# Kernel optimization log

Measured on AMD Instinct MI355X. Metric: run time of the kernel, lower is better.

## Reference

```python
import jax, jax.numpy as jnp
import numpy as np

B, C, W, H = 32, 64, 96, 96
L = 32          # LSTM hidden size
OUT = 256       # conv output channels
EPS = 1e-5


def _lstm_dir(x, wih, whh, b):
    # x: [N, T, D]; wih: [4L, D]; whh: [4L, L]; b: [4L] (b_ih + b_hh)
    N, T, D = x.shape
    Lh = whh.shape[1]
    xg = jnp.einsum('ntd,gd->ntg', x, wih) + b  # precompute input projections

    def step(carry, xg_t):
        h, c = carry
        g = xg_t + h @ whh.T
        i, f, gg, o = jnp.split(g, 4, axis=-1)  # PyTorch gate order i,f,g,o
        i = jax.nn.sigmoid(i)
        f = jax.nn.sigmoid(f)
        gg = jnp.tanh(gg)
        o = jax.nn.sigmoid(o)
        c = f * c + i * gg
        h = o * jnp.tanh(c)
        return (h, c), h

    init = (jnp.zeros((N, Lh), x.dtype), jnp.zeros((N, Lh), x.dtype))
    _, hs = jax.lax.scan(step, init, jnp.swapaxes(xg, 0, 1))
    return jnp.swapaxes(hs, 0, 1)  # [N, T, L]


def _bilstm(x, wih_f, whh_f, bih_f, bhh_f, wih_b, whh_b, bih_b, bhh_b):
    hf = _lstm_dir(x, wih_f, whh_f, bih_f + bhh_f)
    hb = _lstm_dir(x[:, ::-1], wih_b, whh_b, bih_b + bhh_b)[:, ::-1]
    return jnp.concatenate([hf, hb], axis=-1)  # [N, T, 2L]


def setup_inputs() -> dict:
    key = jax.random.key(0)
    ks = jax.random.split(key, 24)
    s1 = 1.0 / np.sqrt(L)
    def u(k, shape):
        return jax.random.uniform(k, shape, jnp.float32, -s1, s1)
    inp = {'x': jax.random.normal(ks[0], (B, C, W, H), jnp.float32)}
    # vertical LSTM: input_size=C
    inp['v_wih_f'] = u(ks[1], (4 * L, C)); inp['v_whh_f'] = u(ks[2], (4 * L, L))
    inp['v_bih_f'] = u(ks[3], (4 * L,));  inp['v_bhh_f'] = u(ks[4], (4 * L,))
    inp['v_wih_b'] = u(ks[5], (4 * L, C)); inp['v_whh_b'] = u(ks[6], (4 * L, L))
    inp['v_bih_b'] = u(ks[7], (4 * L,));  inp['v_bhh_b'] = u(ks[8], (4 * L,))
    # horizontal LSTM: input_size=2L
    inp['h_wih_f'] = u(ks[9], (4 * L, 2 * L)); inp['h_whh_f'] = u(ks[10], (4 * L, L))
    inp['h_bih_f'] = u(ks[11], (4 * L,));      inp['h_bhh_f'] = u(ks[12], (4 * L,))
    inp['h_wih_b'] = u(ks[13], (4 * L, 2 * L)); inp['h_whh_b'] = u(ks[14], (4 * L, L))
    inp['h_bih_b'] = u(ks[15], (4 * L,));       inp['h_bhh_b'] = u(ks[16], (4 * L,))
    # 1x1 conv + BN
    inp['conv_w'] = jax.random.normal(ks[17], (OUT, 2 * L), jnp.float32) * 0.05
    inp['conv_b'] = jnp.zeros((OUT,), jnp.float32)
    inp['bn_g'] = jnp.ones((OUT,), jnp.float32)
    inp['bn_b'] = jnp.zeros((OUT,), jnp.float32)
    return inp


def reference(x, v_wih_f, v_whh_f, v_bih_f, v_bhh_f, v_wih_b, v_whh_b, v_bih_b, v_bhh_b,
              h_wih_f, h_whh_f, h_bih_f, h_bhh_f, h_wih_b, h_whh_b, h_bih_b, h_bhh_b,
              conv_w, conv_b, bn_g, bn_b):
    b, c, w, h = x.shape
    xt = jnp.transpose(x, (0, 3, 2, 1))  # [B, H, W, C] (torch transpose(1,3))
    # vertical pass: for each column w, LSTM over H -> batch all columns at once
    xv = jnp.transpose(xt, (0, 2, 1, 3)).reshape(b * w, h, c)  # [B*W, H, C]
    hv = _bilstm(xv, v_wih_f, v_whh_f, v_bih_f, v_bhh_f,
                 v_wih_b, v_whh_b, v_bih_b, v_bhh_b)            # [B*W, H, 2L]
    v = jnp.transpose(hv.reshape(b, w, h, 2 * L), (0, 2, 1, 3))  # [B, H, W, 2L]
    # horizontal pass: for each row h, LSTM over W -> batch all rows at once
    xh = v.reshape(b * h, w, 2 * L)
    hh = _bilstm(xh, h_wih_f, h_whh_f, h_bih_f, h_bhh_f,
                 h_wih_b, h_whh_b, h_bih_b, h_bhh_b).reshape(b, h, w, 2 * L)
    # stack(dim=3) then transpose(1,2) in torch == [B, 2L, W, H]
    y = jnp.transpose(hh, (0, 3, 2, 1))  # [B, 2L, W, H]
    # 1x1 conv
    y = jnp.einsum('bcwh,oc->bowh', y, conv_w) + conv_b[None, :, None, None]
    # BatchNorm2d (training mode: batch statistics, biased variance)
    mean = jnp.mean(y, axis=(0, 2, 3), keepdims=True)
    var = jnp.mean((y - mean) ** 2, axis=(0, 2, 3), keepdims=True)
    out = (y - mean) * jax.lax.rsqrt(var + EPS)
    out = out * bn_g[None, :, None, None] + bn_b[None, :, None, None]
    return out
```

## Files before the change

kernel.cpp:

```cpp
#include <hip/hip_runtime.h>
#include <stdint.h>

#define DI __device__ __forceinline__

constexpr int Bn = 32, Cc = 64, Wn = 96, Hn = 96, Ln = 32, NG = 128, OUTC = 256;
constexpr int SEQ = 96;
constexpr long long NPIX = (long long)Bn * Wn * Hn;
constexpr int GRAM_BLOCKS = 256;
constexpr int PIX_PER_BLOCK = (int)(NPIX / GRAM_BLOCKS);

typedef __attribute__((ext_vector_type(8))) short bf16x8;
typedef __attribute__((ext_vector_type(4))) float f32x4;

constexpr float LOG2E  = 1.44269504088896340736f;
constexpr float TWOL2E = 2.88539008177792681472f;

DI float exp2_(float x) { return __builtin_amdgcn_exp2f(x); }
DI float rcp_(float x)  { return __builtin_amdgcn_rcpf(x); }
DI float bf2f(unsigned short u) { return __uint_as_float(((unsigned)u) << 16); }
DI unsigned short f2bf(float f) {
    unsigned u = __float_as_uint(f);
    u += 0x7FFFu + ((u >> 16) & 1u);
    return (unsigned short)(u >> 16);
}

__global__ __launch_bounds__(256)
void transpose_x(const float* __restrict__ x, unsigned short* __restrict__ xT)
{
    __shared__ alignas(16) unsigned char xs[96 * 128];
    const int tid = threadIdx.x;
    const int b = blockIdx.x / 96, q = blockIdx.x % 96;
    for (int i = tid; i < 1536; i += 256) {
        int c = i / 24, h4 = i - c * 24;
        float4 v = *(const float4*)(x + (((size_t)b * 64 + c) * 96 + q) * 96 + 4 * h4);
        float vv[4] = {v.x, v.y, v.z, v.w};
#pragma unroll
        for (int j = 0; j < 4; ++j) {
            int h = 4 * h4 + j;
            *(unsigned short*)(xs + h * 128 + ((c * 2) ^ ((h & 7) << 4))) = f2bf(vv[j]);
        }
    }
    __syncthreads();
    unsigned short* ob = xT + (size_t)blockIdx.x * 6144;
    for (int i = tid; i < 768; i += 256) {
        int row = i >> 3, k8 = i & 7;
        bf16x8 p = *(const bf16x8*)(xs + row * 128 + ((k8 * 16) ^ ((row & 7) << 4)));
        *(bf16x8*)(ob + (size_t)i * 8) = p;
    }
}

#define FLOAD(XA, XB, STI)                                                     \
    if ((STI) < 96) {                                                          \
        const int tl_ = dir ? 95 - (STI) : (STI);                              \
        XA = *(const bf16x8*)(xTb + (size_t)tl_ * 64);                         \
        XB = *(const bf16x8*)(xTb + (size_t)tl_ * 64 + 32);                    \
    }

#define PPROJ(XA, XB)                                                          \
    _Pragma("unroll")                                                          \
    for (int g_ = 0; g_ < 4; ++g_) {                                           \
        f32x4 tp_ = __builtin_amdgcn_mfma_f32_16x16x32_bf16(ax0[g_], XA, bc[g_], 0, 0, 0); \
        xac[g_] = __builtin_amdgcn_mfma_f32_16x16x32_bf16(ax1[g_], XB, tp_, 0, 0, 0);      \
    }

#define RSTEP(STI)                                                             \
    {                                                                          \
        const bf16x8 hu = *(const bf16x8*)(hcur + n_ * 80 + rg * 16);          \
        f32x4 ac_[4];                                                          \
        _Pragma("unroll")                                                      \
        for (int g_ = 0; g_ < 4; ++g_)                                         \
            ac_[g_] = __builtin_amdgcn_mfma_f32_16x16x32_bf16(ah[g_], hu, xac[g_], 0, 0, 0); \
        unsigned short hs[4];                                                  \
        _Pragma("unroll")                                                      \
        for (int j = 0; j < 4; ++j) {                                          \
            const float iv = rcp_(1.f + exp2_(-ac_[0][j]));                    \
            const float fv = rcp_(1.f + exp2_(-ac_[1][j]));                    \
            const float gr = rcp_(1.f + exp2_(-ac_[2][j]));                    \
            const float gv = fmaf(2.f, gr, -1.f);                              \
            const float ov = rcp_(1.f + exp2_(-ac_[3][j]));                    \
            cc[j] = fmaf(fv, cc[j], iv * gv);                                  \
            const float r_ = rcp_(exp2_(cc[j] * TWOL2E) + 1.f);                \
            const float t2 = -2.f * ov;                                        \
            hs[j] = f2bf(fmaf(t2, r_, ov));                                    \
        }                                                                      \
        ushort4 hp; hp.x = hs[0]; hp.y = hs[1]; hp.z = hs[2]; hp.w = hs[3];    \
        *(ushort4*)(hnxt + n_ * 80 + wv * 32 + rg * 8) = hp;                   \
        *(ushort4*)optr = hp;                                                  \
        optr += odelta;                                                        \
        __syncthreads();                                                       \
        { unsigned char* t_ = hcur; hcur = hnxt; hnxt = t_; }                  \
    }

template<int VERT>
__global__ __launch_bounds__(128, 1)
void lstm_fused(const unsigned short* __restrict__ xT,
                const float* __restrict__ wih_f, const float* __restrict__ whh_f,
                const float* __restrict__ bih_f, const float* __restrict__ bhh_f,
                const float* __restrict__ wih_b, const float* __restrict__ whh_b,
                const float* __restrict__ bih_b, const float* __restrict__ bhh_b,
                unsigned short* __restrict__ outU)
{
    __shared__ alignas(16) unsigned char hbuf[2][16 * 80];

    const int tid = threadIdx.x;
    const int wv = tid >> 6, lane = tid & 63;
    const int dir = blockIdx.x & 1, group = blockIdx.x >> 1;
    const int n_ = lane & 15, rg = lane >> 4;
    const int chain = group * 16 + n_;
    const int b = group / 6;
    const int q = (group % 6) * 16 + n_;

    const float* wih = dir ? wih_b : wih_f;
    const float* whh = dir ? whh_b : whh_f;
    const float* bih = dir ? bih_b : bih_f;
    const float* bhh = dir ? bhh_b : bhh_f;

    bf16x8 ah[4], ax0[4], ax1[4];
    f32x4 bc[4];
#pragma unroll
    for (int g_ = 0; g_ < 4; ++g_) {
        const int tt = 2 * g_ + wv;
        const float sc = (g_ == 2) ? TWOL2E : LOG2E;
        const float* sh = whh + (size_t)(tt * 16 + n_) * 32 + rg * 8;
        const float* sx = wih + (size_t)(tt * 16 + n_) * 64 + rg * 8;
        float4 h0 = *(const float4*)sh, h1 = *(const float4*)(sh + 4);
        float4 x0 = *(const float4*)sx, x1 = *(const float4*)(sx + 4);
        float4 x2 = *(const float4*)(sx + 32), x3 = *(const float4*)(sx + 36);
        ah[g_][0] = (short)f2bf(sc * h0.x); ah[g_][1] = (short)f2bf(sc * h0.y);
        ah[g_][2] = (short)f2bf(sc * h0.z); ah[g_][3] = (short)f2bf(sc * h0.w);
        ah[g_][4] = (short)f2bf(sc * h1.x); ah[g_][5] = (short)f2bf(sc * h1.y);
        ah[g_][6] = (short)f2bf(sc * h1.z); ah[g_][7] = (short)f2bf(sc * h1.w);
        ax0[g_][0] = (short)f2bf(sc * x0.x); ax0[g_][1] = (short)f2bf(sc * x0.y);
        ax0[g_][2] = (short)f2bf(sc * x0.z); ax0[g_][3] = (short)f2bf(sc * x0.w);
        ax0[g_][4] = (short)f2bf(sc * x1.x); ax0[g_][5] = (short)f2bf(sc * x1.y);
        ax0[g_][6] = (short)f2bf(sc * x1.z); ax0[g_][7] = (short)f2bf(sc * x1.w);
        ax1[g_][0] = (short)f2bf(sc * x2.x); ax1[g_][1] = (short)f2bf(sc * x2.y);
        ax1[g_][2] = (short)f2bf(sc * x2.z); ax1[g_][3] = (short)f2bf(sc * x2.w);
        ax1[g_][4] = (short)f2bf(sc * x3.x); ax1[g_][5] = (short)f2bf(sc * x3.y);
        ax1[g_][6] = (short)f2bf(sc * x3.z); ax1[g_][7] = (short)f2bf(sc * x3.w);
#pragma unroll
        for (int j = 0; j < 4; ++j) {
            const int g = tt * 16 + rg * 4 + j;
            bc[g_][j] = sc * (bih[g] + bhh[g]);
        }
    }

    const unsigned short* xTb = xT + (size_t)chain * 6144 + rg * 8;

    const int t0 = dir ? 95 : 0;
    const size_t o0 = VERT ? ((((size_t)b * 96 + t0) * 96 + q) * 64)
                           : ((((size_t)b * 96 + q) * 96 + t0) * 64);
    unsigned short* optr = outU + o0 + dir * 32 + wv * 16 + rg * 4;
    const ptrdiff_t odelta = (ptrdiff_t)(dir ? -1 : 1) * (VERT ? 6144 : 64);

    for (int i = tid; i < 320; i += 128) ((unsigned*)hbuf[0])[i] = 0u;

    unsigned char* hcur = hbuf[0];
    unsigned char* hnxt = hbuf[1];

    float cc[4] = {0.f, 0.f, 0.f, 0.f};
    f32x4 xac[4];
    bf16x8 xa0, xb0, xa1, xb1, xa2, xb2;
    FLOAD(xa0, xb0, 0)
    FLOAD(xa1, xb1, 1)
    PPROJ(xa0, xb0)
    __syncthreads();

    for (int st = 0; st < 96; st += 3) {
        FLOAD(xa2, xb2, st + 2)
        RSTEP(st)
        PPROJ(xa1, xb1)
        FLOAD(xa0, xb0, st + 3)
        RSTEP(st + 1)
        PPROJ(xa2, xb2)
        FLOAD(xa1, xb1, st + 4)
        RSTEP(st + 2)
        PPROJ(xa0, xb0)
    }
}

__global__ __launch_bounds__(256, 2)
void gram_partial(const unsigned short* __restrict__ hh, float* __restrict__ part)
{
    __shared__ alignas(16) unsigned char xsT[2][64 * 144];
    __shared__ float sumb[16][64];

    const int tid = threadIdx.x;
    const int wv = tid >> 6, lane = tid & 63;
    const int lrow = lane & 15, lkg = lane >> 4;
    const int cq = tid & 15, pr = tid >> 4;

    float csum[4] = {0.f, 0.f, 0.f, 0.f};
    f32x4 acc[4];
#pragma unroll
    for (int n = 0; n < 4; ++n) acc[n] = (f32x4){0.f, 0.f, 0.f, 0.f};

    const size_t pix0 = (size_t)blockIdx.x * PIX_PER_BLOCK;

    for (int tile = 0; tile < PIX_PER_BLOCK / 64; ++tile) {
        unsigned char* Xb = xsT[tile & 1];
#pragma unroll
        for (int r = 0; r < 4; ++r) {
            const int p = pr + r * 16;
            ushort4 v = *(const ushort4*)(hh + (pix0 + (size_t)tile * 64 + p) * 64 + cq * 4);
            csum[0] += bf2f(v.x); csum[1] += bf2f(v.y);
            csum[2] += bf2f(v.z); csum[3] += bf2f(v.w);
            *(unsigned short*)(Xb + (cq * 4 + 0) * 144 + p * 2) = v.x;
            *(unsigned short*)(Xb + (cq * 4 + 1) * 144 + p * 2) = v.y;
            *(unsigned short*)(Xb + (cq * 4 + 2) * 144 + p * 2) = v.z;
            *(unsigned short*)(Xb + (cq * 4 + 3) * 144 + p * 2) = v.w;
        }
        __syncthreads();
#pragma unroll
        for (int kc = 0; kc < 2; ++kc) {
            const int kb = (kc * 32 + lkg * 8) * 2;
            bf16x8 af = *(const bf16x8*)(Xb + (wv * 16 + lrow) * 144 + kb);
#pragma unroll
            for (int n = 0; n < 4; ++n) {
                bf16x8 bf_ = *(const bf16x8*)(Xb + (n * 16 + lrow) * 144 + kb);
                acc[n] = __builtin_amdgcn_mfma_f32_16x16x32_bf16(af, bf_, acc[n], 0, 0, 0);
            }
        }
    }

    *(float4*)&sumb[pr][cq * 4] = (float4){csum[0], csum[1], csum[2], csum[3]};
    __syncthreads();
    float* pb = part + (size_t)blockIdx.x * 4160;
    if (tid < 64) {
        float s = 0.f;
#pragma unroll
        for (int r = 0; r < 16; ++r) s += sumb[r][tid];
        pb[4096 + tid] = s;
    }
#pragma unroll
    for (int n = 0; n < 4; ++n)
#pragma unroll
        for (int r = 0; r < 4; ++r)
            pb[(wv * 16 + lkg * 4 + r) * 64 + n * 16 + lrow] = acc[n][r];
}

__global__ void gram_reduce(const float* __restrict__ part, float* __restrict__ M)
{
    int e = blockIdx.x * 256 + threadIdx.x;
    if (e >= 4160) return;
    double s = 0.0;
    for (int p = 0; p < GRAM_BLOCKS; ++p) s += (double)part[(size_t)p * 4160 + e];
    M[e] = (float)s;
}

__global__ __launch_bounds__(256)
void stats_kernel(const float* __restrict__ M, const float* __restrict__ cw,
                  const float* __restrict__ cb, const float* __restrict__ bg,
                  const float* __restrict__ bb,
                  float* __restrict__ Aout, float* __restrict__ Bout)
{
    __shared__ float Ml[4160];
    const int tid = threadIdx.x;
    for (int e = tid; e < 4160; e += 256) Ml[e] = M[e];
    __syncthreads();
    float wr[64];
#pragma unroll
    for (int c = 0; c < 64; ++c) wr[c] = bf2f(f2bf(cw[tid * 64 + c]));
    float s1 = 0.f;
#pragma unroll
    for (int c = 0; c < 64; ++c) s1 = fmaf(wr[c], Ml[4096 + c], s1);
    float s2 = 0.f;
    for (int c = 0; c < 64; ++c) {
        const float* Mr = &Ml[c * 64];
        float t = 0.f;
#pragma unroll
        for (int d = 0; d < 64; ++d) t = fmaf(wr[d], Mr[d], t);
        s2 = fmaf(wr[c], t, s2);
    }
    const double invN = 1.0 / (double)NPIX;
    double cbo = (double)cb[tid];
    double mu = (double)s1 * invN + cbo;
    double ey2 = (double)s2 * invN + 2.0 * cbo * ((double)s1 * invN) + cbo * cbo;
    double var = ey2 - mu * mu;
    double A = (double)bg[tid] / sqrt(var + 1e-5);
    Aout[tid] = (float)A;
    Bout[tid] = (float)((double)bb[tid] + A * (cbo - mu));
}

__global__ __launch_bounds__(512, 2)
void conv_bn_kernel(const unsigned short* __restrict__ hh, const float* __restrict__ cw,
                    const float* __restrict__ Aarr, const float* __restrict__ Barr,
                    float* __restrict__ out)
{
    __shared__ alignas(16) unsigned char UsB[96 * 128];
    __shared__ alignas(16) unsigned char WtB[256 * 128];

    const int tid = threadIdx.x;
    const int b = blockIdx.x / 96, w = blockIdx.x % 96;

    for (int i4 = tid; i4 < 4096; i4 += 512) {
        int wrow = i4 >> 4, k4 = i4 & 15;
        float4 v = *(const float4*)(cw + (size_t)wrow * 64 + k4 * 4);
        ushort4 p; p.x = f2bf(v.x); p.y = f2bf(v.y); p.z = f2bf(v.z); p.w = f2bf(v.w);
        *(ushort4*)(WtB + wrow * 128 + ((k4 * 8) ^ ((wrow & 7) << 4))) = p;
    }
    for (int i = tid; i < 1536; i += 512) {
        int row = i >> 4, k4 = i & 15;
        ushort4 p = *(const ushort4*)(hh + (((size_t)b * 96 + row) * 96 + w) * 64 + k4 * 4);
        *(ushort4*)(UsB + row * 128 + ((k4 * 8) ^ ((row & 7) << 4))) = p;
    }
    __syncthreads();

    const int wv = tid >> 6, lane = tid & 63;
    const int mbase = (wv >> 2) * 48, nbase = (wv & 3) * 64;
    const int lrow = lane & 15, lk = (lane >> 4) * 8;

    f32x4 acc[3][4];
#pragma unroll
    for (int m = 0; m < 3; ++m)
#pragma unroll
        for (int n = 0; n < 4; ++n)
            acc[m][n] = (f32x4){0.f, 0.f, 0.f, 0.f};

#pragma unroll
    for (int ks = 0; ks < 2; ++ks) {
        const int kb = (ks * 32 + lk) * 2;
        bf16x8 am[3], bn[4];
#pragma unroll
        for (int m = 0; m < 3; ++m) {
            int row = mbase + m * 16 + lrow;
            am[m] = *(const bf16x8*)(UsB + row * 128 + (kb ^ ((row & 7) << 4)));
        }
#pragma unroll
        for (int n = 0; n < 4; ++n) {
            int o = nbase + n * 16 + lrow;
            bn[n] = *(const bf16x8*)(WtB + o * 128 + (kb ^ ((o & 7) << 4)));
        }
#pragma unroll
        for (int m = 0; m < 3; ++m)
#pragma unroll
            for (int n = 0; n < 4; ++n)
                acc[m][n] = __builtin_amdgcn_mfma_f32_16x16x32_bf16(am[m], bn[n], acc[m][n], 0, 0, 0);
    }

    const int hbase0 = (lane >> 4) * 4;
#pragma unroll
    for (int n = 0; n < 4; ++n) {
        const int o = nbase + n * 16 + lrow;
        const float Ao = Aarr[o], Bo = Barr[o];
        float* obase = out + (((size_t)b * 256 + o) * 96 + w) * 96;
#pragma unroll
        for (int m = 0; m < 3; ++m) {
            const int h0 = mbase + m * 16 + hbase0;
            f32x4 res;
            res[0] = fmaf(Ao, acc[m][n][0], Bo);
            res[1] = fmaf(Ao, acc[m][n][1], Bo);
            res[2] = fmaf(Ao, acc[m][n][2], Bo);
            res[3] = fmaf(Ao, acc[m][n][3], Bo);
            __builtin_nontemporal_store(res, (f32x4*)(obase + h0));
        }
    }
}

extern "C" void kernel_launch(void* const* d_in, const int* in_sizes, int n_in,
                              void* d_out, int out_size, void* d_ws, size_t ws_size,
                              hipStream_t stream)
{
    const float* x       = (const float*)d_in[0];
    const float* v_wih_f = (const float*)d_in[1];
    const float* v_whh_f = (const float*)d_in[2];
    const float* v_bih_f = (const float*)d_in[3];
    const float* v_bhh_f = (const float*)d_in[4];
    const float* v_wih_b = (const float*)d_in[5];
    const float* v_whh_b = (const float*)d_in[6];
    const float* v_bih_b = (const float*)d_in[7];
    const float* v_bhh_b = (const float*)d_in[8];
    const float* h_wih_f = (const float*)d_in[9];
    const float* h_whh_f = (const float*)d_in[10];
    const float* h_bih_f = (const float*)d_in[11];
    const float* h_bhh_f = (const float*)d_in[12];
    const float* h_wih_b = (const float*)d_in[13];
    const float* h_whh_b = (const float*)d_in[14];
    const float* h_bih_b = (const float*)d_in[15];
    const float* h_bhh_b = (const float*)d_in[16];
    const float* conv_w  = (const float*)d_in[17];
    const float* conv_b  = (const float*)d_in[18];
    const float* bn_g    = (const float*)d_in[19];
    const float* bn_b    = (const float*)d_in[20];
    float* out = (float*)d_out;

    const size_t v_elems = (size_t)Bn * Hn * Wn * 64;
    unsigned short* v_buf = (unsigned short*)(out + (size_t)out_size) - v_elems;
    unsigned short* xT = (unsigned short*)d_out;
    float* part = (float*)((char*)d_out + (64u << 20));

    unsigned short* hh = (unsigned short*)d_ws;
    char* wsb = (char*)d_ws;
    float* M    = (float*)(wsb + 37748736);
    float* Aarr = M + 4160;
    float* Barr = Aarr + 256;

    transpose_x<<<3072, 256, 0, stream>>>(x, xT);
    lstm_fused<1><<<384, 128, 0, stream>>>(xT, v_wih_f, v_whh_f, v_bih_f, v_bhh_f,
                                           v_wih_b, v_whh_b, v_bih_b, v_bhh_b, v_buf);
    lstm_fused<0><<<384, 128, 0, stream>>>(v_buf, h_wih_f, h_whh_f, h_bih_f, h_bhh_f,
                                           h_wih_b, h_whh_b, h_bih_b, h_bhh_b, hh);
    gram_partial<<<GRAM_BLOCKS, 256, 0, stream>>>(hh, part);
    gram_reduce<<<17, 256, 0, stream>>>(part, M);
    stats_kernel<<<1, 256, 0, stream>>>(M, conv_w, conv_b, bn_g, bn_b, Aarr, Barr);
    conv_bn_kernel<<<3072, 512, 0, stream>>>(hh, conv_w, Aarr, Barr, out);
}
```

Before: 339.2 us.

## Interleave two independent LSTM chain groups per block to hide recurrence latency

Each LSTM block now carries two independent 16-chain groups (A and B) with separate hidden-state LDS buffers, cell states and projection accumulators. The recurrent steps of the two groups are interleaved, and a single barrier serves both. Because the dependent MFMA-to-activation chain of one group can overlap with the other's, the serial latency per step is better hidden and barrier count per chain is halved. The grid shrinks from 384 to 192 blocks, leaving fewer blocks than the MI355X has CUs, and register pressure roughly doubles.

```diff
diff --git a/kernel.cpp b/kernel.cpp
--- a/kernel.cpp
+++ b/kernel.cpp
@@ -49,27 +49,27 @@
     }
 }
 
-#define FLOAD(XA, XB, STI)                                                     \
+#define FLOADU(UN, XA, XB, STI)                                                \
     if ((STI) < 96) {                                                          \
         const int tl_ = dir ? 95 - (STI) : (STI);                              \
-        XA = *(const bf16x8*)(xTb + (size_t)tl_ * 64);                         \
-        XB = *(const bf16x8*)(xTb + (size_t)tl_ * 64 + 32);                    \
-    }
-
-#define PPROJ(XA, XB)                                                          \
+        XA = *(const bf16x8*)(xTb##UN + (size_t)tl_ * 64);                     \
+        XB = *(const bf16x8*)(xTb##UN + (size_t)tl_ * 64 + 32);                \
+    }
+
+#define PPROJ(UN, XA, XB)                                                      \
     _Pragma("unroll")                                                          \
     for (int g_ = 0; g_ < 4; ++g_) {                                           \
         f32x4 tp_ = __builtin_amdgcn_mfma_f32_16x16x32_bf16(ax0[g_], XA, bc[g_], 0, 0, 0); \
-        xac[g_] = __builtin_amdgcn_mfma_f32_16x16x32_bf16(ax1[g_], XB, tp_, 0, 0, 0);      \
-    }
-
-#define RSTEP(STI)                                                             \
+        xac##UN[g_] = __builtin_amdgcn_mfma_f32_16x16x32_bf16(ax1[g_], XB, tp_, 0, 0, 0);  \
+    }
+
+#define RSTEPU(UN)                                                             \
     {                                                                          \
-        const bf16x8 hu = *(const bf16x8*)(hcur + n_ * 80 + rg * 16);          \
+        const bf16x8 hu = *(const bf16x8*)(hcur##UN + n_ * 80 + rg * 16);      \
         f32x4 ac_[4];                                                          \
         _Pragma("unroll")                                                      \
         for (int g_ = 0; g_ < 4; ++g_)                                         \
-            ac_[g_] = __builtin_amdgcn_mfma_f32_16x16x32_bf16(ah[g_], hu, xac[g_], 0, 0, 0); \
+            ac_[g_] = __builtin_amdgcn_mfma_f32_16x16x32_bf16(ah[g_], hu, xac##UN[g_], 0, 0, 0); \
         unsigned short hs[4];                                                  \
         _Pragma("unroll")                                                      \
         for (int j = 0; j < 4; ++j) {                                          \
@@ -78,18 +78,23 @@
             const float gr = rcp_(1.f + exp2_(-ac_[2][j]));                    \
             const float gv = fmaf(2.f, gr, -1.f);                              \
             const float ov = rcp_(1.f + exp2_(-ac_[3][j]));                    \
-            cc[j] = fmaf(fv, cc[j], iv * gv);                                  \
-            const float r_ = rcp_(exp2_(cc[j] * TWOL2E) + 1.f);                \
+            cc##UN[j] = fmaf(fv, cc##UN[j], iv * gv);                          \
+            const float r_ = rcp_(exp2_(cc##UN[j] * TWOL2E) + 1.f);            \
             const float t2 = -2.f * ov;                                        \
             hs[j] = f2bf(fmaf(t2, r_, ov));                                    \
         }                                                                      \
         ushort4 hp; hp.x = hs[0]; hp.y = hs[1]; hp.z = hs[2]; hp.w = hs[3];    \
-        *(ushort4*)(hnxt + n_ * 80 + wv * 32 + rg * 8) = hp;                   \
-        *(ushort4*)optr = hp;                                                  \
-        optr += odelta;                                                        \
-        __syncthreads();                                                       \
-        { unsigned char* t_ = hcur; hcur = hnxt; hnxt = t_; }                  \
-    }
+        *(ushort4*)(hnxt##UN + n_ * 80 + wv * 32 + rg * 8) = hp;               \
+        *(ushort4*)optr##UN = hp;                                              \
+        optr##UN += odelta;                                                    \
+    }
+
+#define STEP_SYNC                                                              \
+    asm volatile("s_waitcnt lgkmcnt(0)" ::: "memory");                         \
+    __builtin_amdgcn_s_barrier();                                              \
+    __builtin_amdgcn_sched_barrier(0);                                         \
+    { unsigned char* t_ = hcurA; hcurA = hnxtA; hnxtA = t_; }                  \
+    { unsigned char* t_ = hcurB; hcurB = hnxtB; hnxtB = t_; }
 
 template<int VERT>
 __global__ __launch_bounds__(128, 1)
@@ -100,15 +105,18 @@
                 const float* __restrict__ bih_b, const float* __restrict__ bhh_b,
                 unsigned short* __restrict__ outU)
 {
-    __shared__ alignas(16) unsigned char hbuf[2][16 * 80];
+    __shared__ alignas(16) unsigned char hbufA[2][16 * 80];
+    __shared__ alignas(16) unsigned char hbufB[2][16 * 80];
 
     const int tid = threadIdx.x;
     const int wv = tid >> 6, lane = tid & 63;
-    const int dir = blockIdx.x & 1, group = blockIdx.x >> 1;
+    const int dir = blockIdx.x & 1, gpair = blockIdx.x >> 1;
     const int n_ = lane & 15, rg = lane >> 4;
-    const int chain = group * 16 + n_;
-    const int b = group / 6;
-    const int q = (group % 6) * 16 + n_;
+
+    const int gA = gpair, gB = gpair + 96;
+    const int chainA = gA * 16 + n_, chainB = gB * 16 + n_;
+    const int bA = gA / 6, qA = (gA % 6) * 16 + n_;
+    const int bB = gB / 6, qB = (gB % 6) * 16 + n_;
 
     const float* wih = dir ? wih_b : wih_f;
     const float* whh = dir ? whh_b : whh_f;
@@ -145,37 +153,62 @@
         }
     }
 
-    const unsigned short* xTb = xT + (size_t)chain * 6144 + rg * 8;
+    const unsigned short* xTbA = xT + (size_t)chainA * 6144 + rg * 8;
+    const unsigned short* xTbB = xT + (size_t)chainB * 6144 + rg * 8;
 
     const int t0 = dir ? 95 : 0;
-    const size_t o0 = VERT ? ((((size_t)b * 96 + t0) * 96 + q) * 64)
-                           : ((((size_t)b * 96 + q) * 96 + t0) * 64);
-    unsigned short* optr = outU + o0 + dir * 32 + wv * 16 + rg * 4;
+    const size_t o0A = VERT ? ((((size_t)bA * 96 + t0) * 96 + qA) * 64)
+                            : ((((size_t)bA * 96 + qA) * 96 + t0) * 64);
+    const size_t o0B = VERT ? ((((size_t)bB * 96 + t0) * 96 + qB) * 64)
+                            : ((((size_t)bB * 96 + qB) * 96 + t0) * 64);
+    unsigned short* optrA = outU + o0A + dir * 32 + wv * 16 + rg * 4;
+    unsigned short* optrB = outU + o0B + dir * 32 + wv * 16 + rg * 4;
     const ptrdiff_t odelta = (ptrdiff_t)(dir ? -1 : 1) * (VERT ? 6144 : 64);
 
-    for (int i = tid; i < 320; i += 128) ((unsigned*)hbuf[0])[i] = 0u;
-
-    unsigned char* hcur = hbuf[0];
-    unsigned char* hnxt = hbuf[1];
-
-    float cc[4] = {0.f, 0.f, 0.f, 0.f};
-    f32x4 xac[4];
-    bf16x8 xa0, xb0, xa1, xb1, xa2, xb2;
-    FLOAD(xa0, xb0, 0)
-    FLOAD(xa1, xb1, 1)
-    PPROJ(xa0, xb0)
+    for (int i = tid; i < 320; i += 128) {
+        ((unsigned*)hbufA[0])[i] = 0u;
+        ((unsigned*)hbufB[0])[i] = 0u;
+    }
+
+    unsigned char* hcurA = hbufA[0]; unsigned char* hnxtA = hbufA[1];
+    unsigned char* hcurB = hbufB[0]; unsigned char* hnxtB = hbufB[1];
+
+    float ccA[4] = {0.f, 0.f, 0.f, 0.f};
+    float ccB[4] = {0.f, 0.f, 0.f, 0.f};
+    f32x4 xacA[4], xacB[4];
+    bf16x8 xaA0, xbA0, xaA1, xbA1, xaA2, xbA2;
+    bf16x8 xaB0, xbB0, xaB1, xbB1, xaB2, xbB2;
+
+    FLOADU(A, xaA0, xbA0, 0) FLOADU(B, xaB0, xbB0, 0)
+    FLOADU(A, xaA1, xbA1, 1) FLOADU(B, xaB1, xbB1, 1)
+    PPROJ(A, xaA0, xbA0)
+    PPROJ(B, xaB0, xbB0)
     __syncthreads();
 
     for (int st = 0; st < 96; st += 3) {
-        FLOAD(xa2, xb2, st + 2)
-        RSTEP(st)
-        PPROJ(xa1, xb1)
-        FLOAD(xa0, xb0, st + 3)
-        RSTEP(st + 1)
-        PPROJ(xa2, xb2)
-        FLOAD(xa1, xb1, st + 4)
-        RSTEP(st + 2)
-        PPROJ(xa0, xb0)
+        FLOADU(A, xaA2, xbA2, st + 2)
+        FLOADU(B, xaB2, xbB2, st + 2)
+        RSTEPU(A)
+        PPROJ(A, xaA1, xbA1)
+        RSTEPU(B)
+        PPROJ(B, xaB1, xbB1)
+        STEP_SYNC
+
+        FLOADU(A, xaA0, xbA0, st + 3)
+        FLOADU(B, xaB0, xbB0, st + 3)
+        RSTEPU(A)
+        PPROJ(A, xaA2, xbA2)
+        RSTEPU(B)
+        PPROJ(B, xaB2, xbB2)
+        STEP_SYNC
+
+        FLOADU(A, xaA1, xbA1, st + 4)
+        FLOADU(B, xaB1, xbB1, st + 4)
+        RSTEPU(A)
+        PPROJ(A, xaA0, xbA0)
+        RSTEPU(B)
+        PPROJ(B, xaB0, xbB0)
+        STEP_SYNC
     }
 }
 
@@ -396,9 +429,9 @@
     float* Barr = Aarr + 256;
 
     transpose_x<<<3072, 256, 0, stream>>>(x, xT);
-    lstm_fused<1><<<384, 128, 0, stream>>>(xT, v_wih_f, v_whh_f, v_bih_f, v_bhh_f,
+    lstm_fused<1><<<192, 128, 0, stream>>>(xT, v_wih_f, v_whh_f, v_bih_f, v_bhh_f,
                                            v_wih_b, v_whh_b, v_bih_b, v_bhh_b, v_buf);
-    lstm_fused<0><<<384, 128, 0, stream>>>(v_buf, h_wih_f, h_whh_f, h_bih_f, h_bhh_f,
+    lstm_fused<0><<<192, 128, 0, stream>>>(v_buf, h_wih_f, h_whh_f, h_bih_f, h_bhh_f,
                                            h_wih_b, h_whh_b, h_bih_b, h_bhh_b, hh);
     gram_partial<<<GRAM_BLOCKS, 256, 0, stream>>>(hh, part);
     gram_reduce<<<17, 256, 0, stream>>>(part, M);
```

New measurement: 357.0 us. 1.05x slower.
